# Kernel tuning notes

Hardware: AMD Instinct MI355X
Metric: run time of the kernel (lower is better)

Reference implementation:

```python
import jax, jax.numpy as jnp
import numpy as np
from jax import lax

B, C, M, TDIM, NUM_TASKS = 4, 128, 6, 64, 1
HL, HH = 128, 64
PROTO_LAMBDA = 5.0

def _gelu(x):
    return jax.nn.gelu(x, approximate=False)

def _lin(x, w, b):
    return x @ w.T + b

def _conv(x, w, b=None, groups=1, pad=0):
    y = lax.conv_general_dilated(x, w, (1, 1), [(pad, pad), (pad, pad)],
                                 feature_group_count=groups,
                                 dimension_numbers=('NCHW', 'OIHW', 'NCHW'))
    if b is not None:
        y = y + b[None, :, None, None]
    return y

def _gn(x, g, b, groups, eps=1e-5):
    Bb, Cc, H, W = x.shape
    xg = x.reshape(Bb, groups, -1)
    mu = xg.mean(-1, keepdims=True)
    var = ((xg - mu) ** 2).mean(-1, keepdims=True)
    xn = ((xg - mu) * lax.rsqrt(var + eps)).reshape(Bb, Cc, H, W)
    return xn * g[None, :, None, None] + b[None, :, None, None]

def _norm(x, axis=-1):
    return x / jnp.maximum(jnp.linalg.norm(x, axis=axis, keepdims=True), 1e-12)

def _resize_ac(x, oh, ow):
    # bilinear resize, align_corners=True (matches F.interpolate)
    Bb, Cc, H, W = x.shape
    def grid(n, o):
        s = jnp.linspace(0.0, float(n - 1), o)
        i0 = jnp.floor(s).astype(jnp.int32)
        i1 = jnp.minimum(i0 + 1, n - 1)
        return i0, i1, (s - i0).astype(x.dtype)
    y0, y1, wy = grid(H, oh)
    x0, x1, wx = grid(W, ow)
    t = x[:, :, y0, :] * (1 - wy)[None, None, :, None] + x[:, :, y1, :] * wy[None, None, :, None]
    return t[:, :, :, x0] * (1 - wx)[None, None, None, :] + t[:, :, :, x1] * wx[None, None, None, :]

def _forward(x_low, x_high, task_emb, pl_w, pl_g, pl_b, ph_w, ph_g, ph_b, fu_w, fu_g, fu_b,
             pi_w1, pi_b1, pi_w2, pi_b2, se_w1, se_b1, se_g, se_be, se_w2, se_b2,
             at_in_w, at_in_b, at_out_w, at_out_b, pf_w, pf_b,
             sr_w1, sr_b1, sr_w2, sr_b2, asw, eg_w1, eg_b1, eg_w2, eg_b2, ewg_w, ewg_b,
             hd_w1, hd_b1, hd_g, hd_be, hd_w2, hd_b2, eis, sim_temp, proto_amp, task_ids):
    H, W = x_low.shape[-2:]
    x_high = _resize_ac(x_high, H, W)
    xl = _gelu(_gn(_conv(x_low, pl_w), pl_g, pl_b, 1))
    xh = _gelu(_gn(_conv(x_high, ph_w), ph_g, ph_b, 1))
    x = _gelu(_gn(_conv(jnp.concatenate([xh, xl], 1), fu_w), fu_g, fu_b, 1))
    Bb = x.shape[0]

    # prototype initialization from task embedding (first sample per task id)
    pinit = _lin(_gelu(_lin(task_emb, pi_w1, pi_b1)), pi_w2, pi_b2).reshape(Bb, 1, 2, C)
    pinit = _norm(pinit, -1)
    table = jnp.stack([pinit[jnp.argmax(task_ids == t)] for t in range(NUM_TASKS)], 0)
    protos = table[task_ids]                      # (B, n_scales=1, 2, C)
    fg = _norm(protos[:, 0, 0], -1)               # (B, C)
    bg = _norm(protos[:, 0, 1], -1)

    # single-scale encoder: grouped 3x3 conv -> GN(4) -> GELU -> 1x1 conv
    sf = _conv(x, se_w1, se_b1, groups=C // 4, pad=1)
    sf = _conv(_gelu(_gn(sf, se_g, se_be, min(4, C))), se_w2, se_b2)
    sfn = _norm(sf, axis=1)
    fused_sim = (jnp.einsum('bchw,bc->bhw', sfn, fg) - jnp.einsum('bchw,bc->bhw', sfn, bg))[:, None]

    # prototype cross-attention: 2 queries attend over HW keys, 4 heads
    feat = sf.reshape(Bb, C, H * W).transpose(0, 2, 1)
    pq = jnp.stack([fg, bg], 1)                   # (B, 2, C)
    wq, wk, wv = jnp.split(at_in_w, 3, 0)
    bq, bk, bv = jnp.split(at_in_b, 3, 0)
    nh, dh = 4, C // 4
    q = (pq @ wq.T + bq).reshape(Bb, 2, nh, dh).transpose(0, 2, 1, 3)
    k = (feat @ wk.T + bk).reshape(Bb, -1, nh, dh).transpose(0, 2, 1, 3)
    v = (feat @ wv.T + bv).reshape(Bb, -1, nh, dh).transpose(0, 2, 1, 3)
    attn = jax.nn.softmax(jnp.einsum('bhqd,bhkd->bhqk', q, k) / jnp.sqrt(jnp.float32(dh)), -1)
    att = jnp.einsum('bhqk,bhkd->bhqd', attn, v).transpose(0, 2, 1, 3).reshape(Bb, 2, C)
    att = att @ at_out_w.T + at_out_b
    fg_a, bg_a = att[:, 0], att[:, 1]
    proto_feat = _lin(jnp.concatenate([fg_a, bg_a, fg_a - bg_a], -1), pf_w, pf_b)

    # scale routing (degenerate for 1 scale but kept faithful)
    tsw = jax.nn.softmax(_lin(_gelu(_lin(task_emb, sr_w1, sr_b1)), sr_w2, sr_b2), -1)
    fsw = tsw * asw[None, :]
    fsw = fsw / fsw.sum(1, keepdims=True)

    # per-sample M-expert 3x3 depthwise kernels blended toward identity
    ek = _lin(_gelu(_lin(proto_feat, eg_w1, eg_b1)), eg_w2, eg_b2).reshape(Bb, M, C, 9)
    id9 = jnp.zeros((C, 9), x.dtype).at[:, 4].set(1.0)
    ek = ek * eis + id9[None, None] * (1 - eis)
    ew = jax.nn.softmax(_lin(proto_feat, ewg_w, ewg_b), -1)  # (B, M)

    x_enh = x * (1 + 0.5 * jax.nn.sigmoid(fused_sim))
    xp = jnp.pad(x_enh, ((0, 0), (0, 0), (1, 1), (1, 1)))
    # unfold(k=3, pad=1): tap order dy-major matches torch unfold's (B, C*9, HW)
    patches = jnp.stack([xp[:, :, dy:dy + H, dx:dx + W] for dy in range(3) for dx in range(3)], 2)  # (B,C,9,H,W)
    # fold expert mixture into a single per-sample per-channel kernel (same math, reassociated)
    w_eff = jnp.einsum('bmcr,bm->bcr', ek, ew)
    y = jnp.einsum('bcr,bcrhw->bchw', w_eff, patches)

    h = _conv(y, hd_w1, hd_b1, groups=C, pad=1)
    logits = _conv(_gelu(_gn(h, hd_g, hd_be, 1)), hd_w2, hd_b2)   # (B, num_tasks, H, W)
    idx = jnp.broadcast_to(task_ids[:, None, None, None], (Bb, 1, H, W))
    logit_task = jnp.take_along_axis(logits, idx, 1)
    sim_scaled = jnp.tanh(fused_sim / (jnp.abs(fused_sim).mean() + 1e-6) / jnp.maximum(sim_temp, 1e-3))
    logit_task = logit_task + PROTO_LAMBDA * proto_amp * sim_scaled
    pred = _resize_ac(logit_task, 512, 512)
    return pred, y, fsw

def setup_inputs():
    ks = iter(jax.random.split(jax.random.key(0), 64))
    f32 = jnp.float32
    def rnd(*s):
        return jax.random.normal(next(ks), s, f32) * 0.02
    d = {}
    d['x_low'] = jax.random.normal(next(ks), (B, 64, HL, HL), f32)
    d['x_high'] = jax.random.normal(next(ks), (B, 128, HH, HH), f32)
    d['task_emb'] = jax.random.normal(next(ks), (B, TDIM), f32)
    d['pl_w'] = rnd(64, 64, 1, 1); d['pl_g'] = jnp.ones(64, f32); d['pl_b'] = jnp.zeros(64, f32)
    d['ph_w'] = rnd(C, 128, 1, 1); d['ph_g'] = jnp.ones(C, f32); d['ph_b'] = jnp.zeros(C, f32)
    d['fu_w'] = rnd(C, C + 64, 1, 1); d['fu_g'] = jnp.ones(C, f32); d['fu_b'] = jnp.zeros(C, f32)
    d['pi_w1'] = rnd(2 * C, TDIM); d['pi_b1'] = jnp.zeros(2 * C, f32)
    d['pi_w2'] = rnd(2 * C, 2 * C); d['pi_b2'] = jnp.zeros(2 * C, f32)
    d['se_w1'] = rnd(C, 4, 3, 3); d['se_b1'] = jnp.zeros(C, f32)
    d['se_g'] = jnp.ones(C, f32); d['se_be'] = jnp.zeros(C, f32)
    d['se_w2'] = rnd(C, C, 1, 1); d['se_b2'] = jnp.zeros(C, f32)
    d['at_in_w'] = rnd(3 * C, C); d['at_in_b'] = jnp.zeros(3 * C, f32)
    d['at_out_w'] = rnd(C, C); d['at_out_b'] = jnp.zeros(C, f32)
    d['pf_w'] = rnd(C, 3 * C); d['pf_b'] = jnp.zeros(C, f32)
    d['sr_w1'] = rnd(2, TDIM); d['sr_b1'] = jnp.zeros(2, f32)
    d['sr_w2'] = rnd(1, 2); d['sr_b2'] = jnp.zeros(1, f32)
    d['asw'] = jnp.ones(1, f32)
    d['eg_w1'] = rnd(2 * C, C); d['eg_b1'] = jnp.zeros(2 * C, f32)
    d['eg_w2'] = rnd(M * C * 9, 2 * C); d['eg_b2'] = jnp.zeros(M * C * 9, f32)
    d['ewg_w'] = rnd(M, C); d['ewg_b'] = jnp.zeros(M, f32)
    d['hd_w1'] = rnd(C, 1, 3, 3); d['hd_b1'] = jnp.zeros(C, f32)
    d['hd_g'] = jnp.ones(C, f32); d['hd_be'] = jnp.zeros(C, f32)
    d['hd_w2'] = rnd(NUM_TASKS, C, 1, 1); d['hd_b2'] = jnp.zeros(NUM_TASKS, f32)
    d['eis'] = jnp.asarray(0.3, f32)
    d['sim_temp'] = jnp.asarray(0.1, f32)
    d['proto_amp'] = jnp.asarray(1.0, f32)
    d['task_ids'] = jnp.zeros((B,), jnp.int32)
    return d

def reference(x_low, x_high, task_emb, pl_w, pl_g, pl_b, ph_w, ph_g, ph_b, fu_w, fu_g, fu_b,
              pi_w1, pi_b1, pi_w2, pi_b2, se_w1, se_b1, se_g, se_be, se_w2, se_b2,
              at_in_w, at_in_b, at_out_w, at_out_b, pf_w, pf_b,
              sr_w1, sr_b1, sr_w2, sr_b2, asw, eg_w1, eg_b1, eg_w2, eg_b2, ewg_w, ewg_b,
              hd_w1, hd_b1, hd_g, hd_be, hd_w2, hd_b2, eis, sim_temp, proto_amp, task_ids):
    return _forward(x_low, x_high, task_emb, pl_w, pl_g, pl_b, ph_w, ph_g, ph_b, fu_w, fu_g, fu_b,
                    pi_w1, pi_b1, pi_w2, pi_b2, se_w1, se_b1, se_g, se_be, se_w2, se_b2,
                    at_in_w, at_in_b, at_out_w, at_out_b, pf_w, pf_b,
                    sr_w1, sr_b1, sr_w2, sr_b2, asw, eg_w1, eg_b1, eg_w2, eg_b2, ewg_w, ewg_b,
                    hd_w1, hd_b1, hd_g, hd_be, hd_w2, hd_b2, eis, sim_temp, proto_amp, task_ids)
```

## Files before the change

### kernel.cpp

```cpp
#include <hip/hip_runtime.h>
#include <math.h>

constexpr int B_ = 4;
constexpr int C_ = 128;
constexpr int HW_ = 16384;
constexpr int W_ = 128;
constexpr int M_ = 6;
constexpr int TDIM_ = 64;
constexpr int NT_ = 1;

static __device__ __forceinline__ float gelu_f(float x){
  return 0.5f * x * (1.0f + erff(x * 0.7071067811865476f));
}
static __device__ __forceinline__ int imin(int a, int b){ return a < b ? a : b; }

static __device__ __forceinline__ float block_reduce_sum256(float v, float* lds){
  int t = threadIdx.x;
  lds[t] = v; __syncthreads();
  for (int s = 128; s > 0; s >>= 1){ if (t < s) lds[t] += lds[t + s]; __syncthreads(); }
  float r = lds[0]; __syncthreads();
  return r;
}

__global__ void k_resize(const float* __restrict__ in, float* __restrict__ out,
                         int BC, int Hi, int Wi, int Ho, int Wo){
  int idx = blockIdx.x * 256 + threadIdx.x;
  int total = BC * Ho * Wo;
  if (idx >= total) return;
  int xo = idx % Wo; int yo = (idx / Wo) % Ho; int bc = idx / (Wo * Ho);
  float sy = (Ho > 1) ? yo * (float)(Hi - 1) / (float)(Ho - 1) : 0.f;
  float sx = (Wo > 1) ? xo * (float)(Wi - 1) / (float)(Wo - 1) : 0.f;
  int y0 = (int)floorf(sy); int y1 = imin(y0 + 1, Hi - 1); float wy = sy - (float)y0;
  int x0 = (int)floorf(sx); int x1 = imin(x0 + 1, Wi - 1); float wx = sx - (float)x0;
  const float* p = in + (size_t)bc * Hi * Wi;
  float a = p[y0 * Wi + x0], b = p[y1 * Wi + x0];
  float c = p[y0 * Wi + x1], d = p[y1 * Wi + x1];
  float t0 = a * (1.f - wy) + b * wy;
  float t1 = c * (1.f - wy) + d * wy;
  out[idx] = t0 * (1.f - wx) + t1 * wx;
}

__global__ void k_resize_stat(const float* __restrict__ in,
                              float* __restrict__ out,
                              float* __restrict__ psum, float* __restrict__ psq){
  int b = blockIdx.x; int y = blockIdx.y;
  int t = threadIdx.x;
  __shared__ float red[256];
  float s = 0.f, ss = 0.f;
  const float SC = 63.f / 127.f;
  for (int k = 0; k < 32; ++k){
    int e = y * 8192 + k * 256 + t;
    int c = e >> 14, p = e & 16383;
    int yo = p >> 7, xo = p & 127;
    float sy = yo * SC, sx = xo * SC;
    int y0 = (int)sy; int y1 = imin(y0 + 1, 63); float wy = sy - (float)y0;
    int x0 = (int)sx; int x1 = imin(x0 + 1, 63); float wx = sx - (float)x0;
    const float* pp = in + ((size_t)b * 128 + c) * 4096;
    float a = pp[y0 * 64 + x0], bb = pp[y1 * 64 + x0];
    float cc = pp[y0 * 64 + x1], d = pp[y1 * 64 + x1];
    float t0 = a * (1.f - wy) + bb * wy;
    float t1 = cc * (1.f - wy) + d * wy;
    float v = t0 * (1.f - wx) + t1 * wx;
    out[((size_t)b * 128 + c) * (size_t)HW_ + p] = v;
    s += v; ss += v * v;
  }
  s = block_reduce_sum256(s, red);
  ss = block_reduce_sum256(ss, red);
  if (t == 0){ psum[b * 256 + y] = s; psq[b * 256 + y] = ss; }
}

__global__ void k_stat2(const float* __restrict__ ps, const float* __restrict__ pq,
                        float* __restrict__ gm, float* __restrict__ gi,
                        int nper, float nelem){
  int idx = blockIdx.x; int t = threadIdx.x;
  __shared__ float l1[128], l2[128];
  float s = 0.f, ss = 0.f;
  for (int i = t; i < nper; i += 128){ s += ps[idx * nper + i]; ss += pq[idx * nper + i]; }
  l1[t] = s; l2[t] = ss; __syncthreads();
  for (int st = 64; st > 0; st >>= 1){
    if (t < st){ l1[t] += l1[t + st]; l2[t] += l2[t + st]; }
    __syncthreads();
  }
  if (t == 0){
    float mu = l1[0] / nelem;
    float var = l2[0] / nelem - mu * mu;
    gm[idx] = mu; gi[idx] = rsqrtf(var + 1e-5f);
  }
}

__global__ void k_stat2_dual(const float* __restrict__ psA, const float* __restrict__ pqA,
                             float* __restrict__ gmA, float* __restrict__ giA, float nelemA,
                             const float* __restrict__ psB, const float* __restrict__ pqB,
                             float* __restrict__ gmB, float* __restrict__ giB, float nelemB){
  int idx = blockIdx.x; int t = threadIdx.x;
  __shared__ float l1[128], l2[128];
  const float* ps; const float* pq; float* gm; float* gi; float nelem; int id2;
  if (idx < 4){ ps = psA; pq = pqA; gm = gmA; gi = giA; nelem = nelemA; id2 = idx; }
  else        { ps = psB; pq = pqB; gm = gmB; gi = giB; nelem = nelemB; id2 = idx - 4; }
  float s = 0.f, ss = 0.f;
  for (int i = t; i < 256; i += 128){ s += ps[id2 * 256 + i]; ss += pq[id2 * 256 + i]; }
  l1[t] = s; l2[t] = ss; __syncthreads();
  for (int st = 64; st > 0; st >>= 1){
    if (t < st){ l1[t] += l1[t + st]; l2[t] += l2[t + st]; }
    __syncthreads();
  }
  if (t == 0){
    float mu = l1[0] / nelem;
    float var = l2[0] / nelem - mu * mu;
    gm[id2] = mu; gi[id2] = rsqrtf(var + 1e-5f);
  }
}

__global__ void k_wtall(const float* __restrict__ ph_w, const float* __restrict__ pl_w,
                        const float* __restrict__ fu_w, const float* __restrict__ se_w2,
                        float* __restrict__ wTph, float* __restrict__ wTpl,
                        float* __restrict__ wTfu, float* __restrict__ wTse){
  int idx = blockIdx.x * 256 + threadIdx.x;
  if (idx < 16384){
    int ci = idx / 128, co = idx % 128;
    wTph[idx] = ph_w[co * 128 + ci];
  } else if (idx < 20480){
    int r = idx - 16384; int ci = r / 64, co = r % 64;
    wTpl[r] = pl_w[co * 64 + ci];
  } else if (idx < 45056){
    int r = idx - 20480; int ci = r / 128, co = r % 128;
    wTfu[r] = fu_w[(size_t)co * 192 + ci];
  } else if (idx < 61440){
    int r = idx - 45056; int ci = r / 128, co = r % 128;
    wTse[r] = se_w2[co * 128 + ci];
  }
}

template<int CO, int CIT, int HWN>
static __device__ __forceinline__ void gemm_body(
    const float* __restrict__ in1, const float* __restrict__ wT,
    float* __restrict__ out, float* __restrict__ psum, float* __restrict__ psq,
    int b, int j0, int slot, float* As, float* Bs, float* red){
  const int tid = threadIdx.x;
  const int tj = tid & 15, tco = tid >> 4;
  constexpr int CPT = CO / 16;
  constexpr int AST = CO + 4;
  float acc[CPT][4];
  #pragma unroll
  for (int i = 0; i < CPT; ++i)
    #pragma unroll
    for (int j = 0; j < 4; ++j) acc[i][j] = 0.f;

  for (int k0 = 0; k0 < CIT; k0 += 16){
    const int kk = tid >> 4;
    if constexpr (CO == 128){
      int co = (tid & 15) * 8;
      const float* wp = &wT[(size_t)(k0 + kk) * CO + co];
      *(float4*)&As[kk * AST + co] = *(const float4*)wp;
      *(float4*)&As[kk * AST + co + 4] = *(const float4*)(wp + 4);
    } else {
      int co = (tid & 15) * 4;
      *(float4*)&As[kk * AST + co] = *(const float4*)&wT[(size_t)(k0 + kk) * CO + co];
    }
    {
      int jj = (tid & 15) * 4;
      int ci = k0 + kk;
      float4 v = *(const float4*)&in1[((size_t)b * CIT + ci) * HWN + j0 + jj];
      *(float4*)&Bs[kk * 68 + jj] = v;
    }
    __syncthreads();
    #pragma unroll
    for (int kkk = 0; kkk < 16; ++kkk){
      float4 bq = *(const float4*)&Bs[kkk * 68 + tj * 4];
      float av[CPT];
      if constexpr (CPT == 8){
        float4 a0 = *(const float4*)&As[kkk * AST + tco * 8];
        float4 a1 = *(const float4*)&As[kkk * AST + tco * 8 + 4];
        av[0] = a0.x; av[1] = a0.y; av[2] = a0.z; av[3] = a0.w;
        av[4] = a1.x; av[5] = a1.y; av[6] = a1.z; av[7] = a1.w;
      } else {
        float4 a0 = *(const float4*)&As[kkk * AST + tco * 4];
        av[0] = a0.x; av[1] = a0.y; av[2] = a0.z; av[3] = a0.w;
      }
      #pragma unroll
      for (int i = 0; i < CPT; ++i){
        acc[i][0] = fmaf(av[i], bq.x, acc[i][0]);
        acc[i][1] = fmaf(av[i], bq.y, acc[i][1]);
        acc[i][2] = fmaf(av[i], bq.z, acc[i][2]);
        acc[i][3] = fmaf(av[i], bq.w, acc[i][3]);
      }
    }
    __syncthreads();
  }
  float s = 0.f, ss = 0.f;
  #pragma unroll
  for (int i = 0; i < CPT; ++i){
    int co = tco * CPT + i;
    float4 o;
    o.x = acc[i][0]; o.y = acc[i][1]; o.z = acc[i][2]; o.w = acc[i][3];
    *(float4*)&out[((size_t)b * CO + co) * HWN + j0 + tj * 4] = o;
    s += o.x + o.y + o.z + o.w;
    ss += o.x * o.x + o.y * o.y + o.z * o.z + o.w * o.w;
  }
  s = block_reduce_sum256(s, red);
  ss = block_reduce_sum256(ss, red);
  if (tid == 0){ psum[slot] = s; psq[slot] = ss; }
}

__global__ __launch_bounds__(256, 4) void k_gemm_dual(
    const float* __restrict__ in_ph, const float* __restrict__ wT_ph,
    float* __restrict__ out_ph, float* __restrict__ psD, float* __restrict__ pqD,
    const float* __restrict__ in_pl, const float* __restrict__ wT_pl,
    float* __restrict__ out_pl, float* __restrict__ psB, float* __restrict__ pqB){
  __shared__ float As[16 * 132];
  __shared__ float Bs[16 * 68];
  __shared__ float red[256];
  int b = blockIdx.x;
  if (blockIdx.y < 64){
    int yb = blockIdx.y;
    gemm_body<128, 128, 4096>(in_ph, wT_ph, out_ph, psD, pqD, b, yb * 64, b * 64 + yb, As, Bs, red);
  } else {
    int yb = blockIdx.y - 64;
    gemm_body<64, 64, 16384>(in_pl, wT_pl, out_pl, psB, pqB, b, yb * 64, b * 256 + yb, As, Bs, red);
  }
}

template<int CO, int CIT>
__global__ __launch_bounds__(256, 4) void k_gemm1x1(
    const float* __restrict__ in1, const float* __restrict__ in2, int CI1,
    const float* __restrict__ wT, const float* __restrict__ bias,
    const float* __restrict__ gm1, const float* __restrict__ gi1,
    const float* __restrict__ ga1, const float* __restrict__ be1, int sh1, int ng1,
    const float* __restrict__ gm2, const float* __restrict__ gi2,
    const float* __restrict__ ga2, const float* __restrict__ be2, int sh2, int ng2,
    float* __restrict__ out, float* __restrict__ psum, float* __restrict__ psq){
  __shared__ float As[16][CO + 4];
  __shared__ float Bs[16][68];
  __shared__ float red[256];
  const int b = blockIdx.x;
  const int j0 = blockIdx.y * 64;
  const int tid = threadIdx.x;
  const int tj = tid & 15, tco = tid >> 4;
  constexpr int CPT = CO / 16;

  float acc[CPT][4];
  #pragma unroll
  for (int i = 0; i < CPT; ++i)
    #pragma unroll
    for (int j = 0; j < 4; ++j) acc[i][j] = 0.f;

  for (int k0 = 0; k0 < CIT; k0 += 16){
    const int kk = tid >> 4;
    if constexpr (CO == 128){
      int co = (tid & 15) * 8;
      const float* wp = &wT[(size_t)(k0 + kk) * CO + co];
      *(float4*)&As[kk][co] = *(const float4*)wp;
      *(float4*)&As[kk][co + 4] = *(const float4*)(wp + 4);
    } else {
      int co = (tid & 15) * 4;
      *(float4*)&As[kk][co] = *(const float4*)&wT[(size_t)(k0 + kk) * CO + co];
    }
    {
      int jj = (tid & 15) * 4;
      int ci = k0 + kk;
      float4 v;
      if (ci < CI1){
        v = *(const float4*)&in1[((size_t)b * CI1 + ci) * HW_ + j0 + jj];
        if (gm1){
          int g = ci >> sh1;
          float rs = gi1[b * ng1 + g];
          float ga = ga1[ci] * rs;
          float be = be1[ci] - gm1[b * ng1 + g] * ga;
          v.x = gelu_f(fmaf(v.x, ga, be)); v.y = gelu_f(fmaf(v.y, ga, be));
          v.z = gelu_f(fmaf(v.z, ga, be)); v.w = gelu_f(fmaf(v.w, ga, be));
        }
      } else {
        int c2 = ci - CI1;
        v = *(const float4*)&in2[((size_t)b * (CIT - CI1) + c2) * HW_ + j0 + jj];
        if (gm2){
          int g = c2 >> sh2;
          float rs = gi2[b * ng2 + g];
          float ga = ga2[c2] * rs;
          float be = be2[c2] - gm2[b * ng2 + g] * ga;
          v.x = gelu_f(fmaf(v.x, ga, be)); v.y = gelu_f(fmaf(v.y, ga, be));
          v.z = gelu_f(fmaf(v.z, ga, be)); v.w = gelu_f(fmaf(v.w, ga, be));
        }
      }
      *(float4*)&Bs[kk][jj] = v;
    }
    __syncthreads();
    #pragma unroll
    for (int kkk = 0; kkk < 16; ++kkk){
      float4 bq = *(const float4*)&Bs[kkk][tj * 4];
      float av[CPT];
      if constexpr (CPT == 8){
        float4 a0 = *(const float4*)&As[kkk][tco * 8];
        float4 a1 = *(const float4*)&As[kkk][tco * 8 + 4];
        av[0] = a0.x; av[1] = a0.y; av[2] = a0.z; av[3] = a0.w;
        av[4] = a1.x; av[5] = a1.y; av[6] = a1.z; av[7] = a1.w;
      } else {
        float4 a0 = *(const float4*)&As[kkk][tco * 4];
        av[0] = a0.x; av[1] = a0.y; av[2] = a0.z; av[3] = a0.w;
      }
      #pragma unroll
      for (int i = 0; i < CPT; ++i){
        acc[i][0] = fmaf(av[i], bq.x, acc[i][0]);
        acc[i][1] = fmaf(av[i], bq.y, acc[i][1]);
        acc[i][2] = fmaf(av[i], bq.z, acc[i][2]);
        acc[i][3] = fmaf(av[i], bq.w, acc[i][3]);
      }
    }
    __syncthreads();
  }
  float s = 0.f, ss = 0.f;
  #pragma unroll
  for (int i = 0; i < CPT; ++i){
    int co = tco * CPT + i;
    float bb = bias ? bias[co] : 0.f;
    float4 o;
    o.x = acc[i][0] + bb; o.y = acc[i][1] + bb;
    o.z = acc[i][2] + bb; o.w = acc[i][3] + bb;
    *(float4*)&out[((size_t)b * CO + co) * HW_ + j0 + tj * 4] = o;
    s += o.x + o.y + o.z + o.w;
    ss += o.x * o.x + o.y * o.y + o.z * o.z + o.w * o.w;
  }
  if (psum){
    s = block_reduce_sum256(s, red);
    ss = block_reduce_sum256(ss, red);
    if (tid == 0){
      psum[b * gridDim.y + blockIdx.y] = s;
      psq [b * gridDim.y + blockIdx.y] = ss;
    }
  }
}

__global__ __launch_bounds__(256) void k_se3(const float* __restrict__ x,
    const float* __restrict__ gm, const float* __restrict__ gi,
    const float* __restrict__ gamma, const float* __restrict__ beta,
    const float* __restrict__ w, const float* __restrict__ bias,
    float* __restrict__ out, float* __restrict__ psum, float* __restrict__ psq){
  __shared__ float xs[4][10][128];
  __shared__ float ws[144];
  __shared__ float wb[4];
  __shared__ float red[256];
  const int bgc = blockIdx.x; const int b = bgc >> 5, gc = bgc & 31;
  const int r0 = blockIdx.y * 8;
  const int tid = threadIdx.x;
  const float mu = gm[b], rs = gi[b];
  for (int ch = 0; ch < 4; ++ch){
    int c = gc * 4 + ch;
    float ga = gamma[c] * rs, be = beta[c] - mu * rs * gamma[c];
    const float* px = x + ((size_t)b * C_ + c) * HW_;
    for (int i = tid; i < 10 * 128; i += 256){
      int rr = i >> 7, cc = i & 127;
      int row = r0 - 1 + rr;
      float v = 0.f;
      if ((unsigned)row < 128u) v = gelu_f(fmaf(px[row * W_ + cc], ga, be));
      xs[ch][rr][cc] = v;
    }
  }
  if (tid < 144) ws[tid] = w[(size_t)(gc * 4) * 36 + tid];
  if (tid < 4)   wb[tid] = bias[gc * 4 + tid];
  __syncthreads();
  const int hf = tid >> 7;
  const int cc = tid & 127;
  float s = 0.f, ss = 0.f;
  for (int co_l = 0; co_l < 4; ++co_l){
    float bb = wb[co_l];
    float a0 = bb, a1 = bb, a2 = bb, a3 = bb;
    #pragma unroll
    for (int cil = 0; cil < 4; ++cil){
      float w9[9];
      #pragma unroll
      for (int i = 0; i < 9; ++i) w9[i] = ws[(co_l * 4 + cil) * 9 + i];
      #pragma unroll
      for (int q = 0; q < 6; ++q){
        int xr = 4 * hf + q;
        float mdl = xs[cil][xr][cc];
        float lft = (cc > 0)   ? xs[cil][xr][cc - 1] : 0.f;
        float rgt = (cc < 127) ? xs[cil][xr][cc + 1] : 0.f;
        if (q <= 2){
          int ky = q;       a0 = fmaf(w9[ky*3], lft, a0); a0 = fmaf(w9[ky*3+1], mdl, a0); a0 = fmaf(w9[ky*3+2], rgt, a0);
        }
        if (q >= 1 && q <= 3){
          int ky = q - 1;   a1 = fmaf(w9[ky*3], lft, a1); a1 = fmaf(w9[ky*3+1], mdl, a1); a1 = fmaf(w9[ky*3+2], rgt, a1);
        }
        if (q >= 2 && q <= 4){
          int ky = q - 2;   a2 = fmaf(w9[ky*3], lft, a2); a2 = fmaf(w9[ky*3+1], mdl, a2); a2 = fmaf(w9[ky*3+2], rgt, a2);
        }
        if (q >= 3){
          int ky = q - 3;   a3 = fmaf(w9[ky*3], lft, a3); a3 = fmaf(w9[ky*3+1], mdl, a3); a3 = fmaf(w9[ky*3+2], rgt, a3);
        }
      }
    }
    float* po = &out[((size_t)b * C_ + gc * 4 + co_l) * HW_ + (r0 + 4 * hf) * W_ + cc];
    po[0]       = a0;
    po[W_]      = a1;
    po[2 * W_]  = a2;
    po[3 * W_]  = a3;
    s += a0 + a1 + a2 + a3;
    ss += a0 * a0 + a1 * a1 + a2 * a2 + a3 * a3;
  }
  s = block_reduce_sum256(s, red);
  ss = block_reduce_sum256(ss, red);
  if (tid == 0){
    int idx = (b * 4 + (gc >> 3)) * 128 + (gc & 7) * 16 + blockIdx.y;
    psum[idx] = s; psq[idx] = ss;
  }
}

__global__ __launch_bounds__(256) void k_ydw(const float* __restrict__ x,
    const float* __restrict__ factor,
    const float* __restrict__ gm, const float* __restrict__ gi,
    const float* __restrict__ gamma, const float* __restrict__ beta,
    const float* __restrict__ w_eff, const float* __restrict__ dw_w,
    const float* __restrict__ dw_b, float* __restrict__ y_out,
    float* __restrict__ h_out, float* __restrict__ psum, float* __restrict__ psq){
  __shared__ float xs[36][128];
  __shared__ float ys[34][128];
  __shared__ float red[256];
  const int bc = blockIdx.x; const int b = bc >> 7, c = bc & 127;
  const int r0 = blockIdx.y * 32;
  const int tid = threadIdx.x;
  const float mu = gm[b], rs = gi[b];
  const float ga = gamma[c] * rs, be = beta[c] - mu * rs * gamma[c];
  const float* px = x + ((size_t)b * C_ + c) * HW_;
  const float* pf = factor + (size_t)b * HW_;
  for (int i = tid; i < 36 * 128; i += 256){
    int rr = i >> 7, cc = i & 127;
    int row = r0 - 2 + rr;
    float v = 0.f;
    if ((unsigned)row < 128u)
      v = gelu_f(fmaf(px[row * W_ + cc], ga, be)) * pf[row * W_ + cc];
    xs[rr][cc] = v;
  }
  __syncthreads();
  float w9[9];
  #pragma unroll
  for (int r = 0; r < 9; ++r) w9[r] = w_eff[b * 1152 + c * 9 + r];
  for (int i = tid; i < 34 * 128; i += 256){
    int rr = i >> 7, cc = i & 127;
    int row = r0 - 1 + rr;
    float acc = 0.f;
    if ((unsigned)row < 128u){
      #pragma unroll
      for (int ky = 0; ky < 3; ++ky){
        #pragma unroll
        for (int kx = 0; kx < 3; ++kx){
          int xc = cc + kx - 1;
          if ((unsigned)xc < 128u) acc += w9[ky * 3 + kx] * xs[rr + ky][xc];
        }
      }
    }
    ys[rr][cc] = acc;
    if (rr >= 1 && rr <= 32)
      y_out[((size_t)b * C_ + c) * HW_ + row * W_ + cc] = acc;
  }
  __syncthreads();
  float wd[9];
  #pragma unroll
  for (int r = 0; r < 9; ++r) wd[r] = dw_w[c * 9 + r];
  const float bb = dw_b[c];
  float s = 0.f, ss = 0.f;
  for (int i = tid; i < 32 * 128; i += 256){
    int rr = i >> 7, cc = i & 127;
    int row = r0 + rr;
    float acc = bb;
    #pragma unroll
    for (int ky = 0; ky < 3; ++ky){
      #pragma unroll
      for (int kx = 0; kx < 3; ++kx){
        int yc = cc + kx - 1;
        if ((unsigned)yc < 128u) acc += wd[ky * 3 + kx] * ys[rr + ky][yc];
      }
    }
    h_out[((size_t)b * C_ + c) * HW_ + row * W_ + cc] = acc;
    s += acc; ss += acc * acc;
  }
  s = block_reduce_sum256(s, red);
  ss = block_reduce_sum256(ss, red);
  if (tid == 0){
    int idx = b * 512 + c * 4 + blockIdx.y;
    psum[idx] = s; psq[idx] = ss;
  }
}

__global__ void k_pinit(const float* __restrict__ temb, const float* __restrict__ w1,
                        const float* __restrict__ b1, const float* __restrict__ w2,
                        const float* __restrict__ b2, float* __restrict__ pinit){
  int b = blockIdx.x; int t = threadIdx.x;
  __shared__ float h1[256], p2[256], nrm[2];
  float acc = b1[t];
  for (int i = 0; i < TDIM_; ++i) acc += temb[b * TDIM_ + i] * w1[t * TDIM_ + i];
  h1[t] = gelu_f(acc); __syncthreads();
  acc = b2[t];
  for (int i = 0; i < 256; ++i) acc += h1[i] * w2[t * 256 + i];
  p2[t] = acc; __syncthreads();
  if (t < 2){
    float s = 0.f;
    for (int c = 0; c < 128; ++c){ float v = p2[t * 128 + c]; s += v * v; }
    nrm[t] = fmaxf(sqrtf(s), 1e-12f);
  }
  __syncthreads();
  pinit[b * 256 + t] = p2[t] / nrm[t / 128];
}

__global__ void k_protos(const float* __restrict__ pinit, const int* __restrict__ task_ids,
                         float* __restrict__ fg, float* __restrict__ bg){
  __shared__ int tbl[NT_];
  __shared__ int src[B_];
  __shared__ float nr[B_ * 2];
  int t = threadIdx.x;
  if (t < NT_){
    int idx = 0;
    for (int b = B_ - 1; b >= 0; --b) if (task_ids[b] == t) idx = b;
    tbl[t] = idx;
  }
  __syncthreads();
  if (t < B_){
    int ti = task_ids[t]; ti = ti < 0 ? 0 : (ti >= NT_ ? NT_ - 1 : ti);
    src[t] = tbl[ti];
  }
  __syncthreads();
  if (t < 2 * B_){
    int b = t / 2, r = t % 2;
    float s = 0.f;
    for (int c = 0; c < 128; ++c){ float v = pinit[src[b] * 256 + r * 128 + c]; s += v * v; }
    nr[t] = fmaxf(sqrtf(s), 1e-12f);
  }
  __syncthreads();
  for (int i = t; i < B_ * 128; i += 256){
    int b = i / 128, c = i % 128;
    fg[i] = pinit[src[b] * 256 + c] / nr[b * 2 + 0];
    bg[i] = pinit[src[b] * 256 + 128 + c] / nr[b * 2 + 1];
  }
}

__global__ void k_qk(const float* __restrict__ fg, const float* __restrict__ bg,
                     const float* __restrict__ at_in_w, const float* __restrict__ at_in_b,
                     float* __restrict__ qkvec, float* __restrict__ kdot){
  int b = blockIdx.x, t = threadIdx.x;
  __shared__ float pq[256], qf[256];
  pq[t] = (t < 128) ? fg[b * 128 + t] : bg[b * 128 + (t - 128)];
  __syncthreads();
  {
    int qi = t / 128, o = t % 128;
    float acc = at_in_b[o];
    const float* wr = at_in_w + (size_t)o * 128;
    for (int c = 0; c < 128; ++c) acc += wr[c] * pq[qi * 128 + c];
    qf[qi * 128 + o] = acc;
  }
  __syncthreads();
  for (int e = t; e < 1024; e += 256){
    int p = e / 128, c = e % 128, qi = p / 4, h = p % 4;
    float acc = 0.f;
    for (int d = 0; d < 32; ++d)
      acc += qf[qi * 128 + h * 32 + d] * at_in_w[(size_t)(128 + h * 32 + d) * 128 + c];
    qkvec[b * 1024 + e] = acc;
  }
  if (t < 8){
    int qi = t / 4, h = t % 4;
    float acc = 0.f;
    for (int d = 0; d < 32; ++d) acc += qf[qi * 128 + h * 32 + d] * at_in_b[128 + h * 32 + d];
    kdot[b * 8 + t] = acc;
  }
}

__global__ __launch_bounds__(256) void k_simscores(const float* __restrict__ sf,
                          const float* __restrict__ fg, const float* __restrict__ bg,
                          const float* __restrict__ qkvec, const float* __restrict__ kdot,
                          float* __restrict__ sim, float* __restrict__ factor,
                          float* __restrict__ scores, float* __restrict__ psim){
  int b = blockIdx.x; int j0 = blockIdx.y * 64;
  int t = threadIdx.x;
  int g = t >> 6, jl = t & 63;
  int j = j0 + jl;
  __shared__ float L[10 * 128];
  __shared__ float part[11 * 256];
  __shared__ float red64[64];
  for (int i = t; i < 1280; i += 256){
    int r = i >> 7, c = i & 127;
    L[i] = (r == 0) ? fg[b * 128 + c]
         : (r == 1) ? bg[b * 128 + c]
                    : qkvec[b * 1024 + (r - 2) * 128 + c];
  }
  __syncthreads();
  const float* p = sf + (size_t)b * C_ * HW_ + j;
  float a0=0,a1=0,q0=0,q1=0,q2=0,q3=0,q4=0,q5=0,q6=0,q7=0,nn=0;
  int c0 = g * 32;
  #pragma unroll 8
  for (int c = c0; c < c0 + 32; ++c){
    float v = p[(size_t)c * HW_];
    nn += v * v;
    a0 += L[c] * v;          a1 += L[128 + c] * v;
    q0 += L[256 + c] * v;    q1 += L[384 + c] * v;
    q2 += L[512 + c] * v;    q3 += L[640 + c] * v;
    q4 += L[768 + c] * v;    q5 += L[896 + c] * v;
    q6 += L[1024 + c] * v;   q7 += L[1152 + c] * v;
  }
  part[0 * 256 + t] = nn;  part[1 * 256 + t] = a0;  part[2 * 256 + t] = a1;
  part[3 * 256 + t] = q0;  part[4 * 256 + t] = q1;  part[5 * 256 + t] = q2;
  part[6 * 256 + t] = q3;  part[7 * 256 + t] = q4;  part[8 * 256 + t] = q5;
  part[9 * 256 + t] = q6;  part[10 * 256 + t] = q7;
  __syncthreads();
  float sv = 0.f;
  if (t < 64){
    float tot[11];
    #pragma unroll
    for (int i = 0; i < 11; ++i)
      tot[i] = part[i * 256 + t] + part[i * 256 + t + 64]
             + part[i * 256 + t + 128] + part[i * 256 + t + 192];
    float inv = 1.f / fmaxf(sqrtf(tot[0]), 1e-12f);
    sv = (tot[1] - tot[2]) * inv;
    sim[b * HW_ + j0 + t] = sv;
    factor[b * HW_ + j0 + t] = 1.f + 0.5f / (1.f + expf(-sv));
    const float scale = 0.17677669529663689f;
    #pragma unroll
    for (int pp = 0; pp < 8; ++pp)
      scores[((size_t)(b * 8 + pp)) * HW_ + j0 + t] = (tot[3 + pp] + kdot[b * 8 + pp]) * scale;
  }
  __syncthreads();
  if (t < 64) red64[t] = fabsf(sv);
  __syncthreads();
  for (int s2 = 32; s2 > 0; s2 >>= 1){
    if (t < s2) red64[t] += red64[t + s2];
    __syncthreads();
  }
  if (t == 0) psim[b * 256 + blockIdx.y] = red64[0];
}

__global__ void k_smpart(const float* __restrict__ scores, float* __restrict__ pm,
                         float* __restrict__ pz){
  __shared__ float lds[256];
  int row = blockIdx.x; int chunk = blockIdx.y;
  const float* p = scores + (size_t)row * HW_ + chunk * 2048;
  float m = -1e30f;
  for (int j = threadIdx.x; j < 2048; j += 256) m = fmaxf(m, p[j]);
  lds[threadIdx.x] = m; __syncthreads();
  for (int s = 128; s > 0; s >>= 1){
    if (threadIdx.x < s) lds[threadIdx.x] = fmaxf(lds[threadIdx.x], lds[threadIdx.x + s]);
    __syncthreads();
  }
  m = lds[0]; __syncthreads();
  float z = 0.f;
  for (int j = threadIdx.x; j < 2048; j += 256) z += expf(p[j] - m);
  z = block_reduce_sum256(z, lds);
  if (threadIdx.x == 0){ pm[row * 8 + chunk] = m; pz[row * 8 + chunk] = z; }
}

__global__ void k_wsum(const float* __restrict__ sf, const float* __restrict__ scores,
                       const float* __restrict__ pm, const float* __restrict__ pz,
                       float* __restrict__ wsum4){
  int bc = blockIdx.x; int b = bc / C_, c = bc % C_;
  int chunk = blockIdx.y;
  __shared__ float lds[8 * 256];
  __shared__ float mr[8], zr[8];
  if (threadIdx.x < 8){
    int r = b * 8 + threadIdx.x;
    float m = -1e30f;
    #pragma unroll
    for (int i = 0; i < 8; ++i) m = fmaxf(m, pm[r * 8 + i]);
    float z = 0.f;
    #pragma unroll
    for (int i = 0; i < 8; ++i) z += pz[r * 8 + i] * expf(pm[r * 8 + i] - m);
    mr[threadIdx.x] = m;
    zr[threadIdx.x] = 1.f / z;
  }
  __syncthreads();
  const float* p = sf + (size_t)bc * HW_;
  const float* sc = scores + (size_t)b * 8 * HW_;
  int j0 = chunk * (HW_ / 4), j1 = j0 + HW_ / 4;
  float acc[8] = {0,0,0,0,0,0,0,0};
  for (int j = j0 + threadIdx.x; j < j1; j += 256){
    float v = p[j];
    #pragma unroll
    for (int pp = 0; pp < 8; ++pp)
      acc[pp] = fmaf(expf(sc[(size_t)pp * HW_ + j] - mr[pp]) * zr[pp], v, acc[pp]);
  }
  #pragma unroll
  for (int pp = 0; pp < 8; ++pp) lds[pp * 256 + threadIdx.x] = acc[pp];
  __syncthreads();
  for (int s = 128; s > 0; s >>= 1){
    if (threadIdx.x < s){
      #pragma unroll
      for (int pp = 0; pp < 8; ++pp) lds[pp * 256 + threadIdx.x] += lds[pp * 256 + threadIdx.x + s];
    }
    __syncthreads();
  }
  if (threadIdx.x < 8)
    wsum4[chunk * 4096 + b * 1024 + threadIdx.x * 128 + c] = lds[threadIdx.x * 256];
}

__global__ void k_small(const float* __restrict__ wsum4, const float* __restrict__ at_in_w,
                        const float* __restrict__ at_in_b, const float* __restrict__ at_out_w,
                        const float* __restrict__ at_out_b, const float* __restrict__ pf_w,
                        const float* __restrict__ pf_b, const float* __restrict__ eg_w1,
                        const float* __restrict__ eg_b1, const float* __restrict__ ewg_w,
                        const float* __restrict__ ewg_b, float* __restrict__ eg1_out,
                        float* __restrict__ ew_out){
  int b = blockIdx.x; int t = threadIdx.x;
  __shared__ float wsl[1024], att[256], ao[256], pf[128], ewl[8];
  for (int i = t; i < 1024; i += 256)
    wsl[i] = wsum4[b * 1024 + i] + wsum4[4096 + b * 1024 + i]
           + wsum4[8192 + b * 1024 + i] + wsum4[12288 + b * 1024 + i];
  __syncthreads();
  {
    int qi = t / 128, o = t % 128, h = o / 32, d = o % 32, p = qi * 4 + h;
    float acc = at_in_b[256 + h * 32 + d];
    const float* wr = at_in_w + (size_t)(256 + h * 32 + d) * 128;
    for (int c = 0; c < 128; ++c) acc += wr[c] * wsl[p * 128 + c];
    att[qi * 128 + o] = acc;
  }
  __syncthreads();
  {
    int qi = t / 128, o = t % 128;
    float acc = at_out_b[o];
    const float* wr = at_out_w + (size_t)o * 128;
    for (int c = 0; c < 128; ++c) acc += wr[c] * att[qi * 128 + c];
    ao[qi * 128 + o] = acc;
  }
  __syncthreads();
  if (t < 128){
    float acc = pf_b[t];
    const float* wr = pf_w + (size_t)t * 384;
    for (int c = 0; c < 128; ++c){
      float fa = ao[c], ba = ao[128 + c];
      acc += wr[c] * fa + wr[128 + c] * ba + wr[256 + c] * (fa - ba);
    }
    pf[t] = acc;
  }
  __syncthreads();
  {
    float acc = eg_b1[t];
    const float* wr = eg_w1 + (size_t)t * 128;
    for (int c = 0; c < 128; ++c) acc += wr[c] * pf[c];
    eg1_out[b * 256 + t] = gelu_f(acc);
  }
  if (t < M_){
    float acc = ewg_b[t];
    const float* wr = ewg_w + (size_t)t * 128;
    for (int c = 0; c < 128; ++c) acc += wr[c] * pf[c];
    ewl[t] = acc;
  }
  __syncthreads();
  if (t == 0){
    float m = -1e30f;
    for (int i = 0; i < M_; ++i) m = fmaxf(m, ewl[i]);
    float z = 0.f;
    for (int i = 0; i < M_; ++i){ ewl[i] = expf(ewl[i] - m); z += ewl[i]; }
    for (int i = 0; i < M_; ++i) ew_out[b * M_ + i] = ewl[i] / z;
  }
}

__global__ void k_weff(const float* __restrict__ eg1, const float* __restrict__ ew,
                       const float* __restrict__ eg_w2, const float* __restrict__ eg_b2,
                       const float* __restrict__ eis_p, float* __restrict__ w_eff){
  int b = blockIdx.x; int cr = blockIdx.y * 256 + threadIdx.x;
  __shared__ float e1[256]; __shared__ float ewl[M_];
  e1[threadIdx.x] = eg1[b * 256 + threadIdx.x];
  if (threadIdx.x < M_) ewl[threadIdx.x] = ew[b * M_ + threadIdx.x];
  __syncthreads();
  if (cr >= C_ * 9) return;
  int c = cr / 9, r = cr % 9;
  float eis = eis_p[0];
  float acc = 0.f;
  for (int m = 0; m < M_; ++m){
    size_t row = ((size_t)m * C_ + c) * 9 + r;
    float v = eg_b2[row];
    const float* wr = eg_w2 + row * 256;
    for (int i = 0; i < 256; ++i) v += wr[i] * e1[i];
    float ekv = v * eis + ((r == 4) ? (1.f - eis) : 0.f);
    acc += ewl[m] * ekv;
  }
  w_eff[b * (C_ * 9) + cr] = acc;
}

__global__ __launch_bounds__(256) void k_logits(const float* __restrict__ h,
                         const float* __restrict__ gmean,
                         const float* __restrict__ ginv, const float* __restrict__ hd_g,
                         const float* __restrict__ hd_be, const float* __restrict__ hd_w2,
                         const float* __restrict__ hd_b2, const int* __restrict__ task_ids,
                         float* __restrict__ logits){
  int b = blockIdx.x; int j0 = blockIdx.y * 64;
  int t = threadIdx.x;
  int g = t >> 6, jl = t & 63;
  int it = task_ids[b]; it = it < 0 ? 0 : (it >= NT_ ? NT_ - 1 : it);
  __shared__ float wg[128], wb[128], w2[128];
  __shared__ float part[256];
  if (t < 128){
    wg[t] = hd_g[t];
    wb[t] = hd_be[t];
    w2[t] = hd_w2[it * C_ + t];
  }
  __syncthreads();
  float mu = gmean[b], rs = ginv[b];
  const float* p = h + (size_t)b * C_ * HW_ + j0 + jl;
  float acc = 0.f;
  int c0 = g * 32;
  #pragma unroll 8
  for (int c = c0; c < c0 + 32; ++c){
    float v = p[(size_t)c * HW_];
    v = (v - mu) * rs * wg[c] + wb[c];
    acc += w2[c] * gelu_f(v);
  }
  part[t] = acc;
  __syncthreads();
  if (t < 64){
    float tot = part[t] + part[t + 64] + part[t + 128] + part[t + 192] + hd_b2[it];
    logits[b * HW_ + j0 + t] = tot;
  }
}

__global__ void k_final(float* __restrict__ logits, const float* __restrict__ sim,
                        const float* __restrict__ psim, const float* __restrict__ sim_temp,
                        const float* __restrict__ proto_amp,
                        const float* __restrict__ asw, float* __restrict__ fsw_out){
  __shared__ float red[256];
  float s = psim[threadIdx.x] + psim[256 + threadIdx.x]
          + psim[512 + threadIdx.x] + psim[768 + threadIdx.x];
  s = block_reduce_sum256(s, red);
  int idx = blockIdx.x * 256 + threadIdx.x;
  float mean = s / (float)(B_ * HW_);
  float denom = mean + 1e-6f;
  float temp = fmaxf(sim_temp[0], 0.001f);
  float v = tanhf(sim[idx] / denom / temp);
  logits[idx] += 5.0f * proto_amp[0] * v;
  if (blockIdx.x == 0 && threadIdx.x < B_){
    float a = 1.0f * asw[0];
    fsw_out[threadIdx.x] = a / a;
  }
}

extern "C" void kernel_launch(void* const* d_in, const int* in_sizes, int n_in,
                              void* d_out, int out_size, void* d_ws, size_t ws_size,
                              hipStream_t stream){
  const float* x_low   = (const float*)d_in[0];
  const float* x_high  = (const float*)d_in[1];
  const float* temb    = (const float*)d_in[2];
  const float* pl_w    = (const float*)d_in[3];
  const float* pl_g    = (const float*)d_in[4];
  const float* pl_b    = (const float*)d_in[5];
  const float* ph_w    = (const float*)d_in[6];
  const float* ph_g    = (const float*)d_in[7];
  const float* ph_b    = (const float*)d_in[8];
  const float* fu_w    = (const float*)d_in[9];
  const float* fu_g    = (const float*)d_in[10];
  const float* fu_b    = (const float*)d_in[11];
  const float* pi_w1   = (const float*)d_in[12];
  const float* pi_b1   = (const float*)d_in[13];
  const float* pi_w2   = (const float*)d_in[14];
  const float* pi_b2   = (const float*)d_in[15];
  const float* se_w1   = (const float*)d_in[16];
  const float* se_b1   = (const float*)d_in[17];
  const float* se_g    = (const float*)d_in[18];
  const float* se_be   = (const float*)d_in[19];
  const float* se_w2   = (const float*)d_in[20];
  const float* se_b2   = (const float*)d_in[21];
  const float* at_in_w = (const float*)d_in[22];
  const float* at_in_b = (const float*)d_in[23];
  const float* at_out_w= (const float*)d_in[24];
  const float* at_out_b= (const float*)d_in[25];
  const float* pf_w    = (const float*)d_in[26];
  const float* pf_b    = (const float*)d_in[27];
  const float* asw     = (const float*)d_in[32];
  const float* eg_w1   = (const float*)d_in[33];
  const float* eg_b1   = (const float*)d_in[34];
  const float* eg_w2   = (const float*)d_in[35];
  const float* eg_b2   = (const float*)d_in[36];
  const float* ewg_w   = (const float*)d_in[37];
  const float* ewg_b   = (const float*)d_in[38];
  const float* hd_w1   = (const float*)d_in[39];
  const float* hd_b1   = (const float*)d_in[40];
  const float* hd_g    = (const float*)d_in[41];
  const float* hd_be   = (const float*)d_in[42];
  const float* hd_w2   = (const float*)d_in[43];
  const float* hd_b2   = (const float*)d_in[44];
  const float* eis     = (const float*)d_in[45];
  const float* sim_temp= (const float*)d_in[46];
  const float* proto_amp=(const float*)d_in[47];
  const int*   task_ids= (const int*)d_in[48];

  float* ws = (float*)d_ws;
  const size_t BIG = (size_t)B_ * C_ * HW_;
  float* S0 = ws;
  float* S1 = ws + BIG;
  float* S2 = ws + 2 * BIG;
  float* scores = ws + 3 * BIG;
  float* sm = scores + (size_t)B_ * 8 * HW_;
  float* sim     = sm;             sm += (size_t)B_ * HW_;
  float* factor  = sm;             sm += (size_t)B_ * HW_;
  float* logitsb = sm;             sm += (size_t)B_ * HW_;
  float* psA = sm; sm += 1024; float* pqA = sm; sm += 1024;
  float* psB = sm; sm += 1024; float* pqB = sm; sm += 1024;
  float* psC = sm; sm += 1024; float* pqC = sm; sm += 1024;
  float* psD = sm; sm += 256;  float* pqD = sm; sm += 256;
  float* ps3 = sm; sm += 2048; float* pq3 = sm; sm += 2048;
  float* psH = sm; sm += 2048; float* pqH = sm; sm += 2048;
  float* gmA = sm; sm += 4;  float* giA = sm; sm += 4;
  float* gmB = sm; sm += 4;  float* giB = sm; sm += 4;
  float* gmC = sm; sm += 4;  float* giC = sm; sm += 4;
  float* gm3 = sm; sm += 16; float* gi3 = sm; sm += 16;
  float* gmH = sm; sm += 4;  float* giH = sm; sm += 4;
  float* pinitb  = sm;             sm += 1024;
  float* fgb     = sm;             sm += 512;
  float* bgb     = sm;             sm += 512;
  float* qkvecb  = sm;             sm += 4096;
  float* kdotb   = sm;             sm += 32;
  float* pmb     = sm;             sm += 256;
  float* pzb     = sm;             sm += 256;
  float* wsum4b  = sm;             sm += 16384;
  float* eg1b    = sm;             sm += 1024;
  float* ewb     = sm;             sm += 32;
  float* weffb   = sm;             sm += 4608;
  float* psimb   = sm;             sm += 1024;
  float* wTph    = sm;             sm += 128 * 128;
  float* wTpl    = sm;             sm += 64 * 64;
  float* wTfu    = sm;             sm += 192 * 128;
  float* wTse    = sm;             sm += 128 * 128;

  float* pred_out = (float*)d_out;
  float* y_out    = pred_out + (size_t)B_ * 512 * 512;
  float* fsw_out  = y_out + BIG;

  dim3 blk(256);
  const float* NF = nullptr;
  float* NFm = nullptr;

  k_wtall<<<240, blk, 0, stream>>>(ph_w, pl_w, fu_w, se_w2, wTph, wTpl, wTfu, wTse);
  k_gemm_dual<<<dim3(B_, 320), blk, 0, stream>>>(x_high, wTph, S0, psD, pqD,
                                                 x_low, wTpl, S2, psB, pqB);
  k_resize_stat<<<dim3(B_, 256), blk, 0, stream>>>(S0, S1, psA, pqA);
  k_stat2_dual<<<8, 128, 0, stream>>>(psA, pqA, gmA, giA, (float)(128 * HW_),
                                      psB, pqB, gmB, giB, (float)(64 * HW_));
  k_gemm1x1<128,192><<<dim3(B_, 256), blk, 0, stream>>>(S1, S2, 128, wTfu, NF,
      gmA,giA,ph_g,ph_b,7,1, gmB,giB,pl_g,pl_b,6,1, S0, psC, pqC);
  k_stat2<<<B_, 128, 0, stream>>>(psC, pqC, gmC, giC, 256, (float)(128 * HW_));
  k_se3<<<dim3(B_ * 32, 16), blk, 0, stream>>>(S0, gmC, giC, fu_g, fu_b,
      se_w1, se_b1, S2, ps3, pq3);
  k_stat2<<<B_ * 4, 128, 0, stream>>>(ps3, pq3, gm3, gi3, 128, (float)(32 * HW_));
  k_gemm1x1<128,128><<<dim3(B_, 256), blk, 0, stream>>>(S2, NF, 128, wTse, se_b2,
      gm3,gi3,se_g,se_be,5,4, NF,NF,NF,NF,0,0, S1, NFm, NFm);
  k_pinit<<<B_, blk, 0, stream>>>(temb, pi_w1, pi_b1, pi_w2, pi_b2, pinitb);
  k_protos<<<1, blk, 0, stream>>>(pinitb, task_ids, fgb, bgb);
  k_qk<<<B_, blk, 0, stream>>>(fgb, bgb, at_in_w, at_in_b, qkvecb, kdotb);
  k_simscores<<<dim3(B_, 256), blk, 0, stream>>>(S1, fgb, bgb, qkvecb, kdotb,
                                                 sim, factor, scores, psimb);
  k_smpart<<<dim3(B_ * 8, 8), blk, 0, stream>>>(scores, pmb, pzb);
  k_wsum<<<dim3(B_ * C_, 4), blk, 0, stream>>>(S1, scores, pmb, pzb, wsum4b);
  k_small<<<B_, blk, 0, stream>>>(wsum4b, at_in_w, at_in_b, at_out_w, at_out_b,
                                  pf_w, pf_b, eg_w1, eg_b1, ewg_w, ewg_b, eg1b, ewb);
  k_weff<<<dim3(B_, 5), blk, 0, stream>>>(eg1b, ewb, eg_w2, eg_b2, eis, weffb);
  k_ydw<<<dim3(B_ * C_, 4), blk, 0, stream>>>(S0, factor, gmC, giC, fu_g, fu_b,
      weffb, hd_w1, hd_b1, y_out, S2, psH, pqH);
  k_stat2<<<B_, 128, 0, stream>>>(psH, pqH, gmH, giH, 512, (float)(128 * HW_));
  k_logits<<<dim3(B_, 256), blk, 0, stream>>>(S2, gmH, giH, hd_g, hd_be, hd_w2, hd_b2,
                                              task_ids, logitsb);
  k_final<<<(unsigned)((size_t)B_ * HW_ / 256), blk, 0, stream>>>(logitsb, sim, psimb,
                                                                  sim_temp, proto_amp,
                                                                  asw, fsw_out);
  k_resize<<<(unsigned)((size_t)B_ * 512 * 512 / 256), blk, 0, stream>>>(logitsb, pred_out,
                                                                          B_, 128, 128, 512, 512);
}
```

Baseline: 420.1 us.

## Run fusion 1x1 conv on bf16 MFMA with hi/lo split precision

Replaces the fp32 SIMT GEMM for the fusion 1x1 conv (192->128 channels) with a kernel built on 16x16x32 bf16 MFMA instructions. It emulates fp32 accuracy by splitting both weights and activations into bf16 high and low parts and issuing three MFMAs per tile. Weights are pre-split and K-permuted in the weight-transform kernel. The kernel keeps the fused groupnorm+GELU input prologue and the per-block stat reduction. Dropping the lo*lo term and using bf16 operands risks small accuracy differences.

```diff
diff --git a/kernel.cpp b/kernel.cpp
--- a/kernel.cpp
+++ b/kernel.cpp
@@ -9,10 +9,25 @@
 constexpr int TDIM_ = 64;
 constexpr int NT_ = 1;
 
+typedef __attribute__((ext_vector_type(8))) short bf16x8;
+typedef __attribute__((ext_vector_type(4))) float f32x4;
+
 static __device__ __forceinline__ float gelu_f(float x){
   return 0.5f * x * (1.0f + erff(x * 0.7071067811865476f));
 }
 static __device__ __forceinline__ int imin(int a, int b){ return a < b ? a : b; }
+static __device__ __forceinline__ unsigned short f2bf(float x){
+  unsigned int u = __float_as_uint(x);
+  unsigned int r = (u + 0x7FFFu + ((u >> 16) & 1u)) >> 16;
+  return (unsigned short)r;
+}
+static __device__ __forceinline__ float bf2f(unsigned short h){
+  return __uint_as_float(((unsigned int)h) << 16);
+}
+static __device__ __forceinline__ int kperm(int k){
+  int kc = k >> 5, r = k & 31;
+  return kc * 32 + ((r & 15) >> 2) * 8 + (r >> 4) * 4 + (r & 3);
+}
 
 static __device__ __forceinline__ float block_reduce_sum256(float v, float* lds){
   int t = threadIdx.x;
@@ -114,7 +129,8 @@
 __global__ void k_wtall(const float* __restrict__ ph_w, const float* __restrict__ pl_w,
                         const float* __restrict__ fu_w, const float* __restrict__ se_w2,
                         float* __restrict__ wTph, float* __restrict__ wTpl,
-                        float* __restrict__ wTfu, float* __restrict__ wTse){
+                        float* __restrict__ wTse,
+                        unsigned short* __restrict__ wHi, unsigned short* __restrict__ wLo){
   int idx = blockIdx.x * 256 + threadIdx.x;
   if (idx < 16384){
     int ci = idx / 128, co = idx % 128;
@@ -122,12 +138,17 @@
   } else if (idx < 20480){
     int r = idx - 16384; int ci = r / 64, co = r % 64;
     wTpl[r] = pl_w[co * 64 + ci];
-  } else if (idx < 45056){
+  } else if (idx < 36864){
     int r = idx - 20480; int ci = r / 128, co = r % 128;
-    wTfu[r] = fu_w[(size_t)co * 192 + ci];
+    wTse[r] = se_w2[co * 128 + ci];
   } else if (idx < 61440){
-    int r = idx - 45056; int ci = r / 128, co = r % 128;
-    wTse[r] = se_w2[co * 128 + ci];
+    int r = idx - 36864;
+    int co = r / 192, k = r % 192;
+    float v = fu_w[r];
+    unsigned short h = f2bf(v);
+    int pos = co * 192 + kperm(k);
+    wHi[pos] = h;
+    wLo[pos] = f2bf(v - bf2f(h));
   }
 }
 
@@ -218,6 +239,104 @@
     int yb = blockIdx.y - 64;
     gemm_body<64, 64, 16384>(in_pl, wT_pl, out_pl, psB, pqB, b, yb * 64, b * 256 + yb, As, Bs, red);
   }
+}
+
+__global__ __launch_bounds__(256) void k_mfu(
+    const float* __restrict__ in1, const float* __restrict__ in2,
+    const unsigned short* __restrict__ wHi, const unsigned short* __restrict__ wLo,
+    const float* __restrict__ gmA, const float* __restrict__ giA,
+    const float* __restrict__ ga1, const float* __restrict__ be1,
+    const float* __restrict__ gmB, const float* __restrict__ giB,
+    const float* __restrict__ ga2, const float* __restrict__ be2,
+    float* __restrict__ out, float* __restrict__ psum, float* __restrict__ psq){
+  __shared__ unsigned short Bhi[64 * 200];
+  __shared__ unsigned short Blo[64 * 200];
+  __shared__ float red[256];
+  const int b = blockIdx.x;
+  const int j0 = blockIdx.y * 64;
+  const int t = threadIdx.x;
+  {
+    const int px = t & 63;
+    const int ci0 = (t >> 6) * 48;
+    const float muA = gmA[b], rsA = giA[b];
+    const float muB = gmB[b], rsB = giB[b];
+    for (int c4 = 0; c4 < 48; c4 += 4){
+      unsigned short ph4[4], pl4[4];
+      int k0 = ci0 + c4;
+      #pragma unroll
+      for (int i2 = 0; i2 < 4; ++i2){
+        int cc = k0 + i2;
+        float v, ga, be;
+        if (cc < 128){
+          v = in1[((size_t)b * 128 + cc) * HW_ + j0 + px];
+          ga = ga1[cc] * rsA; be = be1[cc] - muA * ga;
+        } else {
+          int c2 = cc - 128;
+          v = in2[((size_t)b * 64 + c2) * HW_ + j0 + px];
+          ga = ga2[c2] * rsB; be = be2[c2] - muB * ga;
+        }
+        float x = gelu_f(fmaf(v, ga, be));
+        unsigned short h = f2bf(x);
+        ph4[i2] = h;
+        pl4[i2] = f2bf(x - bf2f(h));
+      }
+      int r0 = k0 & 31;
+      int pos0 = (k0 >> 5) * 32 + ((r0 & 15) >> 2) * 8 + (r0 >> 4) * 4;
+      *(uint2*)&Bhi[px * 200 + pos0] = *(uint2*)ph4;
+      *(uint2*)&Blo[px * 200 + pos0] = *(uint2*)pl4;
+    }
+  }
+  __syncthreads();
+  const int w = t >> 6, lane = t & 63;
+  const int row = lane & 15, kg = lane >> 4;
+  f32x4 acc[2][4];
+  #pragma unroll
+  for (int cf = 0; cf < 2; ++cf)
+    #pragma unroll
+    for (int pf = 0; pf < 4; ++pf) acc[cf][pf] = (f32x4){0.f, 0.f, 0.f, 0.f};
+  for (int kc = 0; kc < 6; ++kc){
+    bf16x8 ah[2], al[2], bh[4], bl[4];
+    #pragma unroll
+    for (int cf = 0; cf < 2; ++cf){
+      int co = w * 32 + cf * 16 + row;
+      size_t wo = (size_t)co * 192 + kc * 32 + kg * 8;
+      ah[cf] = *(const bf16x8*)&wHi[wo];
+      al[cf] = *(const bf16x8*)&wLo[wo];
+    }
+    #pragma unroll
+    for (int pf = 0; pf < 4; ++pf){
+      int px = pf * 16 + row;
+      int bo = px * 200 + kc * 32 + kg * 8;
+      bh[pf] = *(const bf16x8*)&Bhi[bo];
+      bl[pf] = *(const bf16x8*)&Blo[bo];
+    }
+    #pragma unroll
+    for (int cf = 0; cf < 2; ++cf)
+      #pragma unroll
+      for (int pf = 0; pf < 4; ++pf){
+        acc[cf][pf] = __builtin_amdgcn_mfma_f32_16x16x32_bf16(ah[cf], bh[pf], acc[cf][pf], 0, 0, 0);
+        acc[cf][pf] = __builtin_amdgcn_mfma_f32_16x16x32_bf16(ah[cf], bl[pf], acc[cf][pf], 0, 0, 0);
+        acc[cf][pf] = __builtin_amdgcn_mfma_f32_16x16x32_bf16(al[cf], bh[pf], acc[cf][pf], 0, 0, 0);
+      }
+  }
+  float s = 0.f, ss = 0.f;
+  #pragma unroll
+  for (int cf = 0; cf < 2; ++cf){
+    #pragma unroll
+    for (int pf = 0; pf < 4; ++pf){
+      int px = j0 + pf * 16 + row;
+      #pragma unroll
+      for (int i = 0; i < 4; ++i){
+        int co = w * 32 + cf * 16 + kg * 4 + i;
+        float v = acc[cf][pf][i];
+        out[((size_t)b * 128 + co) * HW_ + px] = v;
+        s += v; ss += v * v;
+      }
+    }
+  }
+  s = block_reduce_sum256(s, red);
+  ss = block_reduce_sum256(ss, red);
+  if (t == 0){ psum[b * 256 + blockIdx.y] = s; psq[b * 256 + blockIdx.y] = ss; }
 }
 
 template<int CO, int CIT>
@@ -910,8 +1029,9 @@
   float* psimb   = sm;             sm += 1024;
   float* wTph    = sm;             sm += 128 * 128;
   float* wTpl    = sm;             sm += 64 * 64;
-  float* wTfu    = sm;             sm += 192 * 128;
   float* wTse    = sm;             sm += 128 * 128;
+  unsigned short* wHi = (unsigned short*)sm; sm += 12288;
+  unsigned short* wLo = (unsigned short*)sm; sm += 12288;
 
   float* pred_out = (float*)d_out;
   float* y_out    = pred_out + (size_t)B_ * 512 * 512;
@@ -921,14 +1041,14 @@
   const float* NF = nullptr;
   float* NFm = nullptr;
 
-  k_wtall<<<240, blk, 0, stream>>>(ph_w, pl_w, fu_w, se_w2, wTph, wTpl, wTfu, wTse);
+  k_wtall<<<240, blk, 0, stream>>>(ph_w, pl_w, fu_w, se_w2, wTph, wTpl, wTse, wHi, wLo);
   k_gemm_dual<<<dim3(B_, 320), blk, 0, stream>>>(x_high, wTph, S0, psD, pqD,
                                                  x_low, wTpl, S2, psB, pqB);
   k_resize_stat<<<dim3(B_, 256), blk, 0, stream>>>(S0, S1, psA, pqA);
   k_stat2_dual<<<8, 128, 0, stream>>>(psA, pqA, gmA, giA, (float)(128 * HW_),
                                       psB, pqB, gmB, giB, (float)(64 * HW_));
-  k_gemm1x1<128,192><<<dim3(B_, 256), blk, 0, stream>>>(S1, S2, 128, wTfu, NF,
-      gmA,giA,ph_g,ph_b,7,1, gmB,giB,pl_g,pl_b,6,1, S0, psC, pqC);
+  k_mfu<<<dim3(B_, 256), blk, 0, stream>>>(S1, S2, wHi, wLo,
+      gmA, giA, ph_g, ph_b, gmB, giB, pl_g, pl_b, S0, psC, pqC);
   k_stat2<<<B_, 128, 0, stream>>>(psC, pqC, gmC, giC, 256, (float)(128 * HW_));
   k_se3<<<dim3(B_ * 32, 16), blk, 0, stream>>>(S0, gmC, giC, fu_g, fu_b,
       se_w1, se_b1, S2, ps3, pq3);
```

After: 421.7 us. Within noise of the previous version (+0.4%).
